# Kernel tuning notes

Measured on AMD Instinct MI355X. Metric: run time of the kernel, lower is better.

The kernel has to match this reference:

```python
import jax, jax.numpy as jnp
import numpy as np

D = 1024
H = 16
DEPTH = D // H


def setup_inputs() -> dict:
    key = jax.random.key(0)
    ks = jax.random.split(key, 9)
    s = 1.0 / np.sqrt(D)
    return {
        "x": jax.random.normal(ks[0], (2, 2048, D), dtype=jnp.float32),
        "Wq": jax.random.uniform(ks[1], (D, D), jnp.float32, -s, s),
        "bq": jax.random.uniform(ks[2], (D,), jnp.float32, -s, s),
        "Wk": jax.random.uniform(ks[3], (D, D), jnp.float32, -s, s),
        "bk": jax.random.uniform(ks[4], (D,), jnp.float32, -s, s),
        "Wv": jax.random.uniform(ks[5], (D, D), jnp.float32, -s, s),
        "bv": jax.random.uniform(ks[6], (D,), jnp.float32, -s, s),
        "Wo": jax.random.uniform(ks[7], (D, D), jnp.float32, -s, s),
        "bo": jax.random.uniform(ks[8], (D,), jnp.float32, -s, s),
    }


def _split_heads(t):
    b, s, _ = t.shape
    return t.reshape(b, s, H, DEPTH).transpose(0, 2, 1, 3)  # [B,H,S,depth]


def reference(x, Wq, bq, Wk, bk, Wv, bv, Wo, bo):
    q = _split_heads(x @ Wq.T + bq)
    k = _split_heads(x @ Wk.T + bk)
    v = _split_heads(x @ Wv.T + bv)
    scores = jnp.einsum("bhqd,bhkd->bhqk", q, k) / jnp.sqrt(jnp.float32(DEPTH))
    weights = jax.nn.softmax(scores, axis=-1)
    attn = jnp.einsum("bhqk,bhkd->bhqd", weights, v)
    b, _, s, _ = attn.shape
    attn = attn.transpose(0, 2, 1, 3).reshape(b, s, D)
    return attn @ Wo.T + bo
```

## Files before the change

### kernel.cpp

```cpp
#include <hip/hip_runtime.h>
#include <hip/hip_bf16.h>


typedef __bf16 bf16x8 __attribute__((ext_vector_type(8)));
typedef float f32x4 __attribute__((ext_vector_type(4)));
typedef unsigned short u16;
typedef unsigned short u16x4 __attribute__((ext_vector_type(4)));
typedef unsigned short u16x8 __attribute__((ext_vector_type(8)));
typedef unsigned int u32x2 __attribute__((ext_vector_type(2)));

__device__ __forceinline__ u16 f2bf(float f) {
  union { float f; unsigned u; } x; x.f = f;
  return (u16)((x.u + 0x7fffu + ((x.u >> 16) & 1u)) >> 16);
}

__device__ __forceinline__ void load_lds16(const void* g, void* l) {
  __builtin_amdgcn_global_load_lds((const __attribute__((address_space(1))) void*)g,
                                   (__attribute__((address_space(3))) void*)l,
                                   16, 0, 0);
}

__device__ __forceinline__ bf16x8 frag128(const u16* base, int row, int ch) {
  return *(const bf16x8*)((const char*)base + row * 128 + (((ch) ^ (row & 7)) << 4));
}
__device__ __forceinline__ bf16x8 frag256(const u16* base, int row, int ch) {
  return *(const bf16x8*)((const char*)base + row * 256 + (((ch) ^ (row & 7)) << 4));
}

__device__ __forceinline__ float exp2_hw(float x) {
  float r;
  asm("v_exp_f32 %0, %1" : "=v"(r) : "v"(x));
  return r;
}

__device__ __forceinline__ unsigned cvt_pk_bf16(float lo, float hi) {
  unsigned r;
  asm("v_cvt_pk_bf16_f32 %0, %1, %2" : "=v"(r) : "v"(lo), "v"(hi));
  return r;
}

__global__ __launch_bounds__(256) void cvt_all(
    const float* __restrict__ x, const float* __restrict__ wq,
    const float* __restrict__ wk, const float* __restrict__ wv,
    const float* __restrict__ wo, u16* __restrict__ dst) {
  int i = blockIdx.x * 256 + threadIdx.x;
  const float* src;
  int loc;
  if (i < 1048576) {
    src = x; loc = i;
  } else {
    int j = i - 1048576;
    int seg = j >> 18;
    loc = j & 262143;
    src = (seg == 0) ? wq : (seg == 1) ? wk : (seg == 2) ? wv : wo;
  }
  f32x4 v = ((const f32x4*)src)[loc];
  u16x4 o;
#pragma unroll
  for (int j = 0; j < 4; ++j) o[j] = f2bf(v[j]);
  ((u16x4*)dst)[i] = o;
}

template <int BM, int MODE>
__global__ __launch_bounds__(256) void gemm_bf16(
    const u16* __restrict__ A, const u16* __restrict__ Bw,
    const float* __restrict__ bias0, const float* __restrict__ bias1,
    const float* __restrict__ bias2,
    u16* __restrict__ o_q, u16* __restrict__ o_k, u16* __restrict__ o_vt,
    float* __restrict__ o_f, int K) {
  constexpr int MBF = BM / 32;
  __shared__ u16 sA[BM * 64];
  __shared__ u16 sB[128 * 64];
  const int tid = threadIdx.x, l = tid & 63, w = tid >> 6;
  const int wr = w >> 1, wc = w & 1;
  const int lr = l & 15, lq = l >> 4;
  const int m0 = blockIdx.y * BM, n0 = blockIdx.x * 128;

  f32x4 acc[MBF][4];
#pragma unroll
  for (int mb = 0; mb < MBF; ++mb)
#pragma unroll
    for (int nb = 0; nb < 4; ++nb) acc[mb][nb] = f32x4{0.f, 0.f, 0.f, 0.f};

  const int nkt = K / 64;
  for (int kt = 0; kt < nkt; ++kt) {
#pragma unroll
    for (int i = 0; i < BM / 32; ++i) {
      int p = (i * 4 + w) * 1024 + l * 16;
      int row = p >> 7, ch = ((p >> 4) & 7) ^ (row & 7);
      load_lds16(A + (size_t)(m0 + row) * K + kt * 64 + ch * 8,
                 (char*)sA + (i * 4 + w) * 1024);
    }
#pragma unroll
    for (int i = 0; i < 4; ++i) {
      int p = (i * 4 + w) * 1024 + l * 16;
      int row = p >> 7, ch = ((p >> 4) & 7) ^ (row & 7);
      load_lds16(Bw + (size_t)(n0 + row) * K + kt * 64 + ch * 8,
                 (char*)sB + (i * 4 + w) * 1024);
    }
    __syncthreads();
#pragma unroll
    for (int ks = 0; ks < 2; ++ks) {
      bf16x8 af[MBF], bfr[4];
#pragma unroll
      for (int mb = 0; mb < MBF; ++mb)
        af[mb] = frag128(sA, wr * (BM / 2) + mb * 16 + lr, lq + 4 * ks);
#pragma unroll
      for (int nb = 0; nb < 4; ++nb)
        bfr[nb] = frag128(sB, wc * 64 + nb * 16 + lr, lq + 4 * ks);
#pragma unroll
      for (int mb = 0; mb < MBF; ++mb)
#pragma unroll
        for (int nb = 0; nb < 4; ++nb)
          acc[mb][nb] = __builtin_amdgcn_mfma_f32_16x16x32_bf16(
              af[mb], bfr[nb], acc[mb][nb], 0, 0, 0);
    }
    __syncthreads();
  }

#pragma unroll
  for (int nb = 0; nb < 4; ++nb) {
    const int n = n0 + wc * 64 + nb * 16 + lr;
    if constexpr (MODE == 0) {
      const int qkv = n >> 10, c = n & 1023;
      const float* bp = (qkv == 0) ? bias0 : ((qkv == 1) ? bias1 : bias2);
      const float bv = bp[c];
      const int h = c >> 6, d = c & 63;
      if (qkv == 2) {
#pragma unroll
        for (int mb = 0; mb < MBF; ++mb) {
          int mbase = m0 + wr * (BM / 2) + mb * 16 + lq * 4;
          int b = mbase >> 11, s0 = mbase & 2047;
          u16x4 pk;
#pragma unroll
          for (int r = 0; r < 4; ++r) pk[r] = f2bf(acc[mb][nb][r] + bv);
          *(u16x4*)(o_vt + ((size_t)((b * 16 + h) * 64 + d)) * 2048 + s0) = pk;
        }
      } else {
        u16* dp = (qkv == 0) ? o_q : o_k;
#pragma unroll
        for (int mb = 0; mb < MBF; ++mb)
#pragma unroll
          for (int r = 0; r < 4; ++r) {
            int m = m0 + wr * (BM / 2) + mb * 16 + lq * 4 + r;
            int b = m >> 11, s = m & 2047;
            float v = acc[mb][nb][r] + bv;
            if (qkv == 0) v *= 0.18033688011f;
            dp[((size_t)(b * 16 + h) * 2048 + s) * 64 + d] = f2bf(v);
          }
      }
    } else {
      const float bv = bias0[n];
#pragma unroll
      for (int mb = 0; mb < MBF; ++mb)
#pragma unroll
        for (int r = 0; r < 4; ++r) {
          int m = m0 + wr * (BM / 2) + mb * 16 + lq * 4 + r;
          o_f[(size_t)m * 1024 + n] = acc[mb][nb][r] + bv;
        }
    }
  }
}

__global__ __launch_bounds__(256, 2) void attn_fwd(
    const u16* __restrict__ q16, const u16* __restrict__ k16,
    const u16* __restrict__ vt16, u16* __restrict__ att16) {
  __shared__ u16 sK[2][128 * 64];
  __shared__ u16 sV[2][64 * 128];
  __shared__ u16 sP[4][32 * 64];
  const int tid = threadIdx.x, l = tid & 63, w = tid >> 6;
  const int lr = l & 15, lq = l >> 4;
  const int lin = (blockIdx.y << 4) | blockIdx.x;
  const int wg = (lin & 7) * 64 + (lin >> 3);
  const int qt = wg & 15, bh = wg >> 4;
  const int b = bh >> 4, h = bh & 15;
  const char* kg = (const char*)(k16 + (size_t)bh * 2048 * 64);
  const char* vg = (const char*)(vt16 + (size_t)bh * 64 * 2048);
  char* sPw = (char*)&sP[w][0];
  const int swzP = (lr & 7) << 4;

  bf16x8 aq[2][2];
#pragma unroll
  for (int mb = 0; mb < 2; ++mb)
#pragma unroll
    for (int ks = 0; ks < 2; ++ks) {
      int qrow = qt * 128 + w * 32 + mb * 16 + lr;
      aq[mb][ks] = *(const bf16x8*)(q16 + ((size_t)bh * 2048 + qrow) * 64 +
                                    ks * 32 + lq * 8);
    }

  const int krow0 = tid >> 3, kch = tid & 7;
  const int vrow0 = tid >> 4, vch = tid & 15;

  f32x4 kbuf[4], vbuf[4];
#pragma unroll
  for (int j = 0; j < 4; ++j)
    kbuf[j] = *(const f32x4*)(kg + j * 4096 + tid * 16);
#pragma unroll
  for (int j = 0; j < 4; ++j)
    vbuf[j] = *(const f32x4*)(vg + (size_t)(j * 16 + vrow0) * 4096 + vch * 16);
#pragma unroll
  for (int j = 0; j < 4; ++j) {
    int row = j * 32 + krow0;
    *(f32x4*)((char*)sK[0] + row * 128 + ((kch ^ (row & 7)) << 4)) = kbuf[j];
  }
#pragma unroll
  for (int j = 0; j < 4; ++j) {
    int row = j * 16 + vrow0;
    *(f32x4*)((char*)sV[0] + row * 256 + ((vch ^ (row & 7)) << 4)) = vbuf[j];
  }
#pragma unroll
  for (int j = 0; j < 4; ++j)
    kbuf[j] = *(const f32x4*)(kg + 16384 + j * 4096 + tid * 16);
#pragma unroll
  for (int j = 0; j < 4; ++j)
    vbuf[j] = *(const f32x4*)(vg + (size_t)(j * 16 + vrow0) * 4096 +
                              256 + vch * 16);
  __syncthreads();

  f32x4 o[2][4];
#pragma unroll
  for (int mb = 0; mb < 2; ++mb)
#pragma unroll
    for (int db = 0; db < 4; ++db) o[mb][db] = f32x4{0.f, 0.f, 0.f, 0.f};
  float l_run[2] = {0.f, 0.f};

  for (int kt = 0; kt < 16; ++kt) {
    const int cur = kt & 1;
    const u16* sKc = sK[cur];
    const u16* sVc = sV[cur];

    f32x4 s[2][8];
#pragma unroll
    for (int mb = 0; mb < 2; ++mb)
#pragma unroll
      for (int nb = 0; nb < 8; ++nb) s[mb][nb] = f32x4{0.f, 0.f, 0.f, 0.f};
    __builtin_amdgcn_s_setprio(1);
#pragma unroll
    for (int ks = 0; ks < 2; ++ks) {
#pragma unroll
      for (int g = 0; g < 2; ++g) {
        bf16x8 bk[4];
#pragma unroll
        for (int j = 0; j < 4; ++j)
          bk[j] = frag128(sKc, (g * 4 + j) * 16 + lr, lq + 4 * ks);
#pragma unroll
        for (int j = 0; j < 4; ++j)
#pragma unroll
          for (int mb = 0; mb < 2; ++mb)
            s[mb][g * 4 + j] = __builtin_amdgcn_mfma_f32_16x16x32_bf16(
                bk[j], aq[mb][ks], s[mb][g * 4 + j], 0, 0, 0);
      }
    }
    __builtin_amdgcn_s_setprio(0);

#pragma unroll
    for (int mb = 0; mb < 2; ++mb) {
      float rs = 0.f;
#pragma unroll
      for (int nb = 0; nb < 8; ++nb)
#pragma unroll
        for (int r = 0; r < 4; ++r) {
          float p_ = exp2_hw(s[mb][nb][r]);
          s[mb][nb][r] = p_;
          rs += p_;
        }
      l_run[mb] += rs;
    }

#pragma unroll
    for (int hf = 0; hf < 2; ++hf) {
#pragma unroll
      for (int mb = 0; mb < 2; ++mb) {
        int qrow = mb * 16 + lr;
#pragma unroll
        for (int nb2 = 0; nb2 < 4; ++nb2) {
          u32x2 pk;
          pk[0] = cvt_pk_bf16(s[mb][hf * 4 + nb2][0], s[mb][hf * 4 + nb2][1]);
          pk[1] = cvt_pk_bf16(s[mb][hf * 4 + nb2][2], s[mb][hf * 4 + nb2][3]);
          *(u32x2*)(sPw + qrow * 128 + ((nb2 * 32 + lq * 8) ^ swzP)) = pk;
        }
      }
      __builtin_amdgcn_s_setprio(1);
#pragma unroll
      for (int c2 = 0; c2 < 2; ++c2) {
        bf16x8 ap[2], bv[4];
#pragma unroll
        for (int mb = 0; mb < 2; ++mb)
          ap[mb] = *(const bf16x8*)(sPw + (mb * 16 + lr) * 128 +
                                    ((c2 * 64 + lq * 16) ^ swzP));
#pragma unroll
        for (int db = 0; db < 4; ++db)
          bv[db] = frag256(sVc, db * 16 + lr, (hf * 2 + c2) * 4 + lq);
#pragma unroll
        for (int db = 0; db < 4; ++db)
#pragma unroll
          for (int mb = 0; mb < 2; ++mb)
            o[mb][db] = __builtin_amdgcn_mfma_f32_16x16x32_bf16(
                ap[mb], bv[db], o[mb][db], 0, 0, 0);
      }
      __builtin_amdgcn_s_setprio(0);
    }

    if (kt < 15) {
      u16* sKn = sK[cur ^ 1];
      u16* sVn = sV[cur ^ 1];
#pragma unroll
      for (int j = 0; j < 4; ++j) {
        int row = j * 32 + krow0;
        *(f32x4*)((char*)sKn + row * 128 + ((kch ^ (row & 7)) << 4)) = kbuf[j];
      }
#pragma unroll
      for (int j = 0; j < 4; ++j) {
        int row = j * 16 + vrow0;
        *(f32x4*)((char*)sVn + row * 256 + ((vch ^ (row & 7)) << 4)) = vbuf[j];
      }
      if (kt < 14) {
#pragma unroll
        for (int j = 0; j < 4; ++j)
          kbuf[j] = *(const f32x4*)(kg + (size_t)(kt + 2) * 16384 +
                                    j * 4096 + tid * 16);
#pragma unroll
        for (int j = 0; j < 4; ++j)
          vbuf[j] = *(const f32x4*)(vg + (size_t)(j * 16 + vrow0) * 4096 +
                                    (kt + 2) * 256 + vch * 16);
      }
    }
    __syncthreads();
  }

#pragma unroll
  for (int mb = 0; mb < 2; ++mb) {
    float lv = l_run[mb];
    lv += __shfl_xor(lv, 16, 64);
    lv += __shfl_xor(lv, 32, 64);
    float inv[4];
#pragma unroll
    for (int r = 0; r < 4; ++r) inv[r] = 1.f / __shfl(lv, lq * 4 + r, 64);
#pragma unroll
    for (int db = 0; db < 4; ++db)
#pragma unroll
      for (int r = 0; r < 4; ++r) {
        float v = o[mb][db][r] * inv[r];
        int qg_ = qt * 128 + w * 32 + mb * 16 + lq * 4 + r;
        int col = h * 64 + db * 16 + lr;
        att16[((size_t)(b * 2048 + qg_)) * 1024 + col] = f2bf(v);
      }
  }
}

extern "C" void kernel_launch(void* const* d_in, const int* in_sizes, int n_in,
                              void* d_out, int out_size, void* d_ws, size_t ws_size,
                              hipStream_t stream) {
  const float* x  = (const float*)d_in[0];
  const float* Wq = (const float*)d_in[1];
  const float* bq = (const float*)d_in[2];
  const float* Wk = (const float*)d_in[3];
  const float* bk = (const float*)d_in[4];
  const float* Wv = (const float*)d_in[5];
  const float* bv = (const float*)d_in[6];
  const float* Wo = (const float*)d_in[7];
  const float* bo = (const float*)d_in[8];
  float* out = (float*)d_out;

  char* ws = (char*)d_ws;
  const size_t MB = 1024 * 1024;
  if (ws_size < 40 * MB) return;
  u16* x16  = (u16*)(ws);
  u16* w16  = (u16*)(ws + 8 * MB);
  u16* q16  = (u16*)(ws + 16 * MB);
  u16* k16  = (u16*)(ws + 24 * MB);
  u16* vt16 = (u16*)(ws + 32 * MB);
  u16* att16 = x16;

  cvt_all<<<8192, 256, 0, stream>>>(x, Wq, Wk, Wv, Wo, x16);

  gemm_bf16<128, 0><<<dim3(24, 32), 256, 0, stream>>>(
      x16, w16, bq, bk, bv, q16, k16, vt16, nullptr, 1024);

  attn_fwd<<<dim3(16, 32), 256, 0, stream>>>(q16, k16, vt16, att16);

  gemm_bf16<64, 1><<<dim3(8, 64), 256, 0, stream>>>(
      att16, w16 + 3145728, bo, nullptr, nullptr, nullptr, nullptr, nullptr,
      out, 1024);
}
```

Baseline: 114.9 us.

## Load V fragments directly from global into registers, dropping V LDS staging

The attention kernel no longer stages the transposed V tile through double-buffered shared memory. Each wave now loads its own MFMA B-operand fragments for V straight from global memory at the top of every key tile, and the PV product is restructured into two explicit halves. This removes the LDS writes, reads and shared-memory footprint for V, which could raise occupancy. In exchange, each of the four waves re-reads the same V data from global/L2, and those loads are issued in the same iteration they are used rather than prefetched two tiles ahead, so their latency is exposed.

```diff
diff --git a/kernel.cpp b/kernel.cpp
--- a/kernel.cpp
+++ b/kernel.cpp
@@ -22,9 +22,6 @@
 
 __device__ __forceinline__ bf16x8 frag128(const u16* base, int row, int ch) {
   return *(const bf16x8*)((const char*)base + row * 128 + (((ch) ^ (row & 7)) << 4));
-}
-__device__ __forceinline__ bf16x8 frag256(const u16* base, int row, int ch) {
-  return *(const bf16x8*)((const char*)base + row * 256 + (((ch) ^ (row & 7)) << 4));
 }
 
 __device__ __forceinline__ float exp2_hw(float x) {
@@ -166,7 +163,6 @@
     const u16* __restrict__ q16, const u16* __restrict__ k16,
     const u16* __restrict__ vt16, u16* __restrict__ att16) {
   __shared__ u16 sK[2][128 * 64];
-  __shared__ u16 sV[2][64 * 128];
   __shared__ u16 sP[4][32 * 64];
   const int tid = threadIdx.x, l = tid & 63, w = tid >> 6;
   const int lr = l & 15, lq = l >> 4;
@@ -190,32 +186,20 @@
     }
 
   const int krow0 = tid >> 3, kch = tid & 7;
-  const int vrow0 = tid >> 4, vch = tid & 15;
-
-  f32x4 kbuf[4], vbuf[4];
+  const char* vfrag = vg + (size_t)lr * 4096 + lq * 16;
+
+  f32x4 kbuf[4];
 #pragma unroll
   for (int j = 0; j < 4; ++j)
     kbuf[j] = *(const f32x4*)(kg + j * 4096 + tid * 16);
-#pragma unroll
-  for (int j = 0; j < 4; ++j)
-    vbuf[j] = *(const f32x4*)(vg + (size_t)(j * 16 + vrow0) * 4096 + vch * 16);
 #pragma unroll
   for (int j = 0; j < 4; ++j) {
     int row = j * 32 + krow0;
     *(f32x4*)((char*)sK[0] + row * 128 + ((kch ^ (row & 7)) << 4)) = kbuf[j];
   }
 #pragma unroll
-  for (int j = 0; j < 4; ++j) {
-    int row = j * 16 + vrow0;
-    *(f32x4*)((char*)sV[0] + row * 256 + ((vch ^ (row & 7)) << 4)) = vbuf[j];
-  }
-#pragma unroll
   for (int j = 0; j < 4; ++j)
     kbuf[j] = *(const f32x4*)(kg + 16384 + j * 4096 + tid * 16);
-#pragma unroll
-  for (int j = 0; j < 4; ++j)
-    vbuf[j] = *(const f32x4*)(vg + (size_t)(j * 16 + vrow0) * 4096 +
-                              256 + vch * 16);
   __syncthreads();
 
   f32x4 o[2][4];
@@ -228,7 +212,16 @@
   for (int kt = 0; kt < 16; ++kt) {
     const int cur = kt & 1;
     const u16* sKc = sK[cur];
-    const u16* sVc = sV[cur];
+
+    bf16x8 v0[4], v1[4], v2[4], v3[4];
+#pragma unroll
+    for (int db = 0; db < 4; ++db) {
+      const char* p = vfrag + (size_t)db * 65536 + kt * 256;
+      v0[db] = *(const bf16x8*)(p);
+      v1[db] = *(const bf16x8*)(p + 64);
+      v2[db] = *(const bf16x8*)(p + 128);
+      v3[db] = *(const bf16x8*)(p + 192);
+    }
 
     f32x4 s[2][8];
 #pragma unroll
@@ -269,61 +262,91 @@
     }
 
 #pragma unroll
-    for (int hf = 0; hf < 2; ++hf) {
-#pragma unroll
-      for (int mb = 0; mb < 2; ++mb) {
-        int qrow = mb * 16 + lr;
-#pragma unroll
-        for (int nb2 = 0; nb2 < 4; ++nb2) {
-          u32x2 pk;
-          pk[0] = cvt_pk_bf16(s[mb][hf * 4 + nb2][0], s[mb][hf * 4 + nb2][1]);
-          pk[1] = cvt_pk_bf16(s[mb][hf * 4 + nb2][2], s[mb][hf * 4 + nb2][3]);
-          *(u32x2*)(sPw + qrow * 128 + ((nb2 * 32 + lq * 8) ^ swzP)) = pk;
-        }
-      }
-      __builtin_amdgcn_s_setprio(1);
-#pragma unroll
-      for (int c2 = 0; c2 < 2; ++c2) {
-        bf16x8 ap[2], bv[4];
+    for (int mb = 0; mb < 2; ++mb) {
+      int qrow = mb * 16 + lr;
+#pragma unroll
+      for (int nb2 = 0; nb2 < 4; ++nb2) {
+        u32x2 pk;
+        pk[0] = cvt_pk_bf16(s[mb][nb2][0], s[mb][nb2][1]);
+        pk[1] = cvt_pk_bf16(s[mb][nb2][2], s[mb][nb2][3]);
+        *(u32x2*)(sPw + qrow * 128 + ((nb2 * 32 + lq * 8) ^ swzP)) = pk;
+      }
+    }
+    __builtin_amdgcn_s_setprio(1);
+    {
+      bf16x8 ap[2];
+#pragma unroll
+      for (int mb = 0; mb < 2; ++mb)
+        ap[mb] = *(const bf16x8*)(sPw + (mb * 16 + lr) * 128 +
+                                  ((0 * 64 + lq * 16) ^ swzP));
+#pragma unroll
+      for (int db = 0; db < 4; ++db)
 #pragma unroll
         for (int mb = 0; mb < 2; ++mb)
-          ap[mb] = *(const bf16x8*)(sPw + (mb * 16 + lr) * 128 +
-                                    ((c2 * 64 + lq * 16) ^ swzP));
-#pragma unroll
-        for (int db = 0; db < 4; ++db)
-          bv[db] = frag256(sVc, db * 16 + lr, (hf * 2 + c2) * 4 + lq);
-#pragma unroll
-        for (int db = 0; db < 4; ++db)
-#pragma unroll
-          for (int mb = 0; mb < 2; ++mb)
-            o[mb][db] = __builtin_amdgcn_mfma_f32_16x16x32_bf16(
-                ap[mb], bv[db], o[mb][db], 0, 0, 0);
-      }
-      __builtin_amdgcn_s_setprio(0);
-    }
+          o[mb][db] = __builtin_amdgcn_mfma_f32_16x16x32_bf16(
+              ap[mb], v0[db], o[mb][db], 0, 0, 0);
+#pragma unroll
+      for (int mb = 0; mb < 2; ++mb)
+        ap[mb] = *(const bf16x8*)(sPw + (mb * 16 + lr) * 128 +
+                                  ((1 * 64 + lq * 16) ^ swzP));
+#pragma unroll
+      for (int db = 0; db < 4; ++db)
+#pragma unroll
+        for (int mb = 0; mb < 2; ++mb)
+          o[mb][db] = __builtin_amdgcn_mfma_f32_16x16x32_bf16(
+              ap[mb], v1[db], o[mb][db], 0, 0, 0);
+    }
+    __builtin_amdgcn_s_setprio(0);
+
+#pragma unroll
+    for (int mb = 0; mb < 2; ++mb) {
+      int qrow = mb * 16 + lr;
+#pragma unroll
+      for (int nb2 = 0; nb2 < 4; ++nb2) {
+        u32x2 pk;
+        pk[0] = cvt_pk_bf16(s[mb][4 + nb2][0], s[mb][4 + nb2][1]);
+        pk[1] = cvt_pk_bf16(s[mb][4 + nb2][2], s[mb][4 + nb2][3]);
+        *(u32x2*)(sPw + qrow * 128 + ((nb2 * 32 + lq * 8) ^ swzP)) = pk;
+      }
+    }
+    __builtin_amdgcn_s_setprio(1);
+    {
+      bf16x8 ap[2];
+#pragma unroll
+      for (int mb = 0; mb < 2; ++mb)
+        ap[mb] = *(const bf16x8*)(sPw + (mb * 16 + lr) * 128 +
+                                  ((0 * 64 + lq * 16) ^ swzP));
+#pragma unroll
+      for (int db = 0; db < 4; ++db)
+#pragma unroll
+        for (int mb = 0; mb < 2; ++mb)
+          o[mb][db] = __builtin_amdgcn_mfma_f32_16x16x32_bf16(
+              ap[mb], v2[db], o[mb][db], 0, 0, 0);
+#pragma unroll
+      for (int mb = 0; mb < 2; ++mb)
+        ap[mb] = *(const bf16x8*)(sPw + (mb * 16 + lr) * 128 +
+                                  ((1 * 64 + lq * 16) ^ swzP));
+#pragma unroll
+      for (int db = 0; db < 4; ++db)
+#pragma unroll
+        for (int mb = 0; mb < 2; ++mb)
+          o[mb][db] = __builtin_amdgcn_mfma_f32_16x16x32_bf16(
+              ap[mb], v3[db], o[mb][db], 0, 0, 0);
+    }
+    __builtin_amdgcn_s_setprio(0);
 
     if (kt < 15) {
       u16* sKn = sK[cur ^ 1];
-      u16* sVn = sV[cur ^ 1];
 #pragma unroll
       for (int j = 0; j < 4; ++j) {
         int row = j * 32 + krow0;
         *(f32x4*)((char*)sKn + row * 128 + ((kch ^ (row & 7)) << 4)) = kbuf[j];
       }
-#pragma unroll
-      for (int j = 0; j < 4; ++j) {
-        int row = j * 16 + vrow0;
-        *(f32x4*)((char*)sVn + row * 256 + ((vch ^ (row & 7)) << 4)) = vbuf[j];
-      }
       if (kt < 14) {
 #pragma unroll
         for (int j = 0; j < 4; ++j)
           kbuf[j] = *(const f32x4*)(kg + (size_t)(kt + 2) * 16384 +
                                     j * 4096 + tid * 16);
-#pragma unroll
-        for (int j = 0; j < 4; ++j)
-          vbuf[j] = *(const f32x4*)(vg + (size_t)(j * 16 + vrow0) * 4096 +
-                                    (kt + 2) * 256 + vch * 16);
       }
     }
     __syncthreads();
```

Measured after the change: 137.0 us. +19.2%, slower.

## Feed softmax probabilities to PV MFMA directly from registers, drop LDS staging

Applied to the files above, without the earlier changes.

The P tile is no longer written to a per-wave LDS buffer and read back. Instead the score-MFMA accumulator layout is packed straight into bf16x8 A-operands, and the V fragments are gathered with matching permuted 8-byte LDS reads so the k-dimension ordering stays consistent. This removes the P round trip through LDS, the LDS write/read latency, and 16KB of shared memory. In exchange, the V reads become two 8-byte loads per fragment instead of one 16-byte load, and these may bank-conflict.

```diff
diff --git a/kernel.cpp b/kernel.cpp
--- a/kernel.cpp
+++ b/kernel.cpp
@@ -23,9 +23,6 @@
 __device__ __forceinline__ bf16x8 frag128(const u16* base, int row, int ch) {
   return *(const bf16x8*)((const char*)base + row * 128 + (((ch) ^ (row & 7)) << 4));
 }
-__device__ __forceinline__ bf16x8 frag256(const u16* base, int row, int ch) {
-  return *(const bf16x8*)((const char*)base + row * 256 + (((ch) ^ (row & 7)) << 4));
-}
 
 __device__ __forceinline__ float exp2_hw(float x) {
   float r;
@@ -37,6 +34,13 @@
   unsigned r;
   asm("v_cvt_pk_bf16_f32 %0, %1, %2" : "=v"(r) : "v"(lo), "v"(hi));
   return r;
+}
+
+__device__ __forceinline__ bf16x8 mk8(unsigned a, unsigned b, unsigned c,
+                                      unsigned d) {
+  union { unsigned u[4]; bf16x8 v; } x;
+  x.u[0] = a; x.u[1] = b; x.u[2] = c; x.u[3] = d;
+  return x.v;
 }
 
 __global__ __launch_bounds__(256) void cvt_all(
@@ -167,7 +171,6 @@
     const u16* __restrict__ vt16, u16* __restrict__ att16) {
   __shared__ u16 sK[2][128 * 64];
   __shared__ u16 sV[2][64 * 128];
-  __shared__ u16 sP[4][32 * 64];
   const int tid = threadIdx.x, l = tid & 63, w = tid >> 6;
   const int lr = l & 15, lq = l >> 4;
   const int lin = (blockIdx.y << 4) | blockIdx.x;
@@ -176,8 +179,6 @@
   const int b = bh >> 4, h = bh & 15;
   const char* kg = (const char*)(k16 + (size_t)bh * 2048 * 64);
   const char* vg = (const char*)(vt16 + (size_t)bh * 64 * 2048);
-  char* sPw = (char*)&sP[w][0];
-  const int swzP = (lr & 7) << 4;
 
   bf16x8 aq[2][2];
 #pragma unroll
@@ -269,36 +270,33 @@
     }
 
 #pragma unroll
-    for (int hf = 0; hf < 2; ++hf) {
-#pragma unroll
-      for (int mb = 0; mb < 2; ++mb) {
-        int qrow = mb * 16 + lr;
-#pragma unroll
-        for (int nb2 = 0; nb2 < 4; ++nb2) {
-          u32x2 pk;
-          pk[0] = cvt_pk_bf16(s[mb][hf * 4 + nb2][0], s[mb][hf * 4 + nb2][1]);
-          pk[1] = cvt_pk_bf16(s[mb][hf * 4 + nb2][2], s[mb][hf * 4 + nb2][3]);
-          *(u32x2*)(sPw + qrow * 128 + ((nb2 * 32 + lq * 8) ^ swzP)) = pk;
-        }
+    for (int g = 0; g < 4; ++g) {
+      bf16x8 ap[2];
+#pragma unroll
+      for (int mb = 0; mb < 2; ++mb)
+        ap[mb] = mk8(cvt_pk_bf16(s[mb][2 * g][0], s[mb][2 * g][1]),
+                     cvt_pk_bf16(s[mb][2 * g][2], s[mb][2 * g][3]),
+                     cvt_pk_bf16(s[mb][2 * g + 1][0], s[mb][2 * g + 1][1]),
+                     cvt_pk_bf16(s[mb][2 * g + 1][2], s[mb][2 * g + 1][3]));
+      bf16x8 bv[4];
+#pragma unroll
+      for (int db = 0; db < 4; ++db) {
+        int row = db * 16 + lr;
+        const char* rb = (const char*)sVc + row * 256;
+        int sw = row & 7;
+        u32x2 lo = *(const u32x2*)(rb + ((((4 * g + (lq >> 1)) ^ sw) << 4) +
+                                         8 * (lq & 1)));
+        u32x2 hi = *(const u32x2*)(rb + ((((4 * g + 2 + (lq >> 1)) ^ sw) << 4) +
+                                         8 * (lq & 1)));
+        bv[db] = mk8(lo[0], lo[1], hi[0], hi[1]);
       }
       __builtin_amdgcn_s_setprio(1);
 #pragma unroll
-      for (int c2 = 0; c2 < 2; ++c2) {
-        bf16x8 ap[2], bv[4];
+      for (int db = 0; db < 4; ++db)
 #pragma unroll
         for (int mb = 0; mb < 2; ++mb)
-          ap[mb] = *(const bf16x8*)(sPw + (mb * 16 + lr) * 128 +
-                                    ((c2 * 64 + lq * 16) ^ swzP));
-#pragma unroll
-        for (int db = 0; db < 4; ++db)
-          bv[db] = frag256(sVc, db * 16 + lr, (hf * 2 + c2) * 4 + lq);
-#pragma unroll
-        for (int db = 0; db < 4; ++db)
-#pragma unroll
-          for (int mb = 0; mb < 2; ++mb)
-            o[mb][db] = __builtin_amdgcn_mfma_f32_16x16x32_bf16(
-                ap[mb], bv[db], o[mb][db], 0, 0, 0);
-      }
+          o[mb][db] = __builtin_amdgcn_mfma_f32_16x16x32_bf16(
+              ap[mb], bv[db], o[mb][db], 0, 0, 0);
       __builtin_amdgcn_s_setprio(0);
     }
 
```

New measurement: 113.7 us. Within noise of the previous version (-1.1%).
